# Performance work log

Measured on AMD Instinct MI355X. Metric: run time of the kernel, lower is better.

The kernel has to match this reference:

```python
import jax, jax.numpy as jnp
import numpy as np

T, B, I, H = 512, 128, 512, 1024


def setup_inputs() -> dict:
    key = jax.random.key(0)
    ks = jax.random.split(key, 9)
    stdv = 1.0 / np.sqrt(H).astype(np.float32)
    u = lambda k, shape: jax.random.uniform(k, shape, jnp.float32, -stdv, stdv)
    return {
        "x": jax.random.normal(ks[0], (T, B, I), jnp.float32),
        "Wf": u(ks[1], (H, H + I)), "bf": u(ks[2], (H,)),
        "Wi": u(ks[3], (H, H + I)), "bi": u(ks[4], (H,)),
        "Wc": u(ks[5], (H, H + I)), "bc": u(ks[6], (H,)),
        "Wo": u(ks[7], (H, H + I)), "bo": u(ks[8], (H,)),
    }


def reference(x, Wf, bf, Wi, bi, Wc, bc, Wo, bo):
    # Single-layer unidirectional LSTM (colah equations), scan over time.
    hidden = Wf.shape[0]
    batch = x.shape[1]

    def step(carry, xt):
        h, c = carry
        z = jnp.concatenate([h, xt], axis=-1)          # (B, H+I)
        f = jax.nn.sigmoid(z @ Wf.T + bf)              # forget gate
        i = jax.nn.sigmoid(z @ Wi.T + bi)              # input gate
        c_tilde = jnp.tanh(z @ Wc.T + bc)              # candidate cell
        o = jax.nn.sigmoid(z @ Wo.T + bo)              # output gate
        c_new = f * c + i * c_tilde
        h_new = o * jnp.tanh(c_new)
        return (h_new, c_new), h_new

    h0 = jnp.zeros((batch, hidden), x.dtype)
    c0 = jnp.zeros((batch, hidden), x.dtype)
    (_, _), hs = jax.lax.scan(step, (h0, c0), x)       # hs: (T, B, H)
    return hs
```

## Files before the change

### kernel.cpp

```cpp
#include <hip/hip_runtime.h>
#include <hip/hip_fp16.h>

#define TSTEPS 512
#define NB 128
#define NI 512
#define HID 1024
#define NWGS 256

typedef _Float16 __attribute__((ext_vector_type(8))) half8;
typedef float __attribute__((ext_vector_type(16))) floatx16;
typedef float __attribute__((ext_vector_type(4))) float4v;
typedef unsigned __attribute__((ext_vector_type(4))) uint4v;

#define WPACK_OFF 0
#define HB0_OFF   12582912
#define HB1_OFF   12845056
#define BAR_OFF   13107200

#define LDS_PBUF  98304
#define LDS_HSH   135168
#define LDS_TOTAL 137728

__device__ __forceinline__ short f2h(float f) {
  _Float16 h = (_Float16)f;
  return *reinterpret_cast<short*>(&h);
}

__device__ __forceinline__ half8 pack8(float4v a, float4v b) {
  half8 r;
  r[0] = (_Float16)a[0]; r[1] = (_Float16)a[1]; r[2] = (_Float16)a[2]; r[3] = (_Float16)a[3];
  r[4] = (_Float16)b[0]; r[5] = (_Float16)b[1]; r[6] = (_Float16)b[2]; r[7] = (_Float16)b[3];
  return r;
}

__device__ __forceinline__ float sigf(float x) { return 1.f / (1.f + __expf(-x)); }

__device__ __forceinline__ uint4v cp_load4(const unsigned* p) {
  uint4v v;
  asm volatile("global_load_dwordx4 %0, %1, off sc0 sc1" : "=v"(v) : "v"(p) : "memory");
  asm volatile("s_waitcnt vmcnt(0)" ::: "memory");
  return v;
}
__device__ __forceinline__ void cp_store(unsigned* p, unsigned v) {
  asm volatile("global_store_dword %0, %1, off sc0 sc1" :: "v"(p), "v"(v) : "memory");
}
__device__ __forceinline__ unsigned long long sys_load_u64(const unsigned long long* p) {
  return __hip_atomic_load(p, __ATOMIC_RELAXED, __HIP_MEMORY_SCOPE_SYSTEM);
}

__global__ void pack_w(const float* __restrict__ Wf, const float* __restrict__ Wi,
                       const float* __restrict__ Wc, const float* __restrict__ Wo,
                       _Float16* __restrict__ wpack) {
  int idx = blockIdx.x * 256 + threadIdx.x;
  if (idx >= 128 * 96 * 64) return;
  int lane = idx & 63;
  int rest = idx >> 6;
  int kt = rest % 96;
  int hs = rest / 96;
  int n = lane & 31, q = lane >> 5;
  int j = n >> 2, g = n & 3;
  int row = hs * 8 + j;
  int k = kt * 16 + q * 8;
  const float* W = (g == 0) ? Wf : (g == 1) ? Wi : (g == 2) ? Wc : Wo;
  const float* src = W + (size_t)row * 1536 + k;
  _Float16* dst = wpack + (size_t)idx * 8;
  #pragma unroll
  for (int e = 0; e < 8; e++) dst[e] = (_Float16)src[e];
}

__global__ void zero_h(unsigned* __restrict__ hb0, unsigned* __restrict__ bar) {
  int i = blockIdx.x * 256 + threadIdx.x;
  if (i < 65536)
    __hip_atomic_store(&hb0[i], 0u, __ATOMIC_RELAXED, __HIP_MEMORY_SCOPE_SYSTEM);
  if (i < 512)
    __hip_atomic_store(&bar[i], 0u, __ATOMIC_RELAXED, __HIP_MEMORY_SCOPE_SYSTEM);
}

__global__ void __launch_bounds__(256, 1)
lstm_main(const float* __restrict__ x,
          const float* __restrict__ bfv, const float* __restrict__ biv,
          const float* __restrict__ bcv, const float* __restrict__ bov,
          const _Float16* __restrict__ wpack,
          _Float16* __restrict__ hb0, _Float16* __restrict__ hb1,
          unsigned* __restrict__ bar, float* __restrict__ out) {
  extern __shared__ char lds[];
  short* wlds = (short*)lds;
  float* pbuf = (float*)(lds + LDS_PBUF);
  float* hshare = (float*)(lds + LDS_HSH);

  const int tid = threadIdx.x;
  const int lane = tid & 63;
  const int wv = tid >> 6;
  const int hs = blockIdx.x & 127;
  const int mh = blockIdx.x >> 7;

  {
    const uint4* src = (const uint4*)wpack + (size_t)hs * 6144;
    uint4* dst = (uint4*)wlds;
    #pragma unroll
    for (int i = 0; i < 24; i++) dst[i * 256 + tid] = src[i * 256 + tid];
  }

  const int rj = tid & 7;
  const int rm4 = tid >> 3;
  float rbias[4] = {0.f, 0.f, 0.f, 0.f};
  float cstate[4] = {0.f, 0.f, 0.f, 0.f};
  if (tid < 128) {
    int hg = hs * 8 + rj;
    rbias[0] = bfv[hg]; rbias[1] = biv[hg]; rbias[2] = bcv[hg]; rbias[3] = bov[hg];
  }

  const int n32 = lane & 31;
  const int q = lane >> 5;

  __syncthreads();

  for (int t = 0; t < TSTEPS; t++) {
    const _Float16* hrd = (t & 1) ? hb1 : hb0;
    _Float16* hwr = (t & 1) ? hb0 : hb1;

    floatx16 acc0, acc1;
    #pragma unroll
    for (int i = 0; i < 16; i++) { acc0[i] = 0.f; acc1[i] = 0.f; }

    {
      const float* xbase = x + (size_t)t * NB * NI;
      const int r0 = (mh * 2 + 0) * 32 + n32;
      #pragma unroll
      for (int kk = 0; kk < 8; kk++) {
        int xt = wv * 8 + kk;
        half8 bfrag = *(const half8*)(wlds + ((64 + xt) * 64 + lane) * 8);
        const float* xs = xbase + xt * 16 + q * 8;
        float4v xa0 = *(const float4v*)(xs + (size_t)r0 * NI);
        float4v xb0 = *(const float4v*)(xs + (size_t)r0 * NI + 4);
        float4v xa1 = *(const float4v*)(xs + (size_t)(r0 + 32) * NI);
        float4v xb1 = *(const float4v*)(xs + (size_t)(r0 + 32) * NI + 4);
        acc0 = __builtin_amdgcn_mfma_f32_32x32x16_f16(pack8(xa0, xb0), bfrag, acc0, 0, 0, 0);
        acc1 = __builtin_amdgcn_mfma_f32_32x32x16_f16(pack8(xa1, xb1), bfrag, acc1, 0, 0, 0);
      }
    }

    if (t > 0) {
      const unsigned need = (unsigned)t;
      if (tid < 32) {
        const unsigned* p = bar + mh * 128 + tid * 4;
        for (;;) {
          uint4v v = cp_load4(p);
          int ok = (v[0] >= need) & (v[1] >= need) & (v[2] >= need) & (v[3] >= need);
          unsigned long long b = __ballot(ok);
          if ((unsigned)b == 0xFFFFFFFFu) break;
          __builtin_amdgcn_s_sleep(2);
        }
      }
      __syncthreads();
    }

    {
      const char* hp = (const char*)hrd + ((size_t)mh << 17);
      #pragma unroll
      for (int ph = 0; ph < 2; ph++) {
        unsigned long long w[8][4];
        #pragma unroll
        for (int kk = 0; kk < 8; kk++) {
          int ht = wv * 16 + ph * 8 + kk;
          const unsigned long long* hq =
              (const unsigned long long*)(hp + (((ht * 2 + q) << 10) | (n32 << 4)));
          w[kk][0] = sys_load_u64(hq + 0);
          w[kk][1] = sys_load_u64(hq + 1);
          w[kk][2] = sys_load_u64(hq + 64);
          w[kk][3] = sys_load_u64(hq + 65);
        }
        #pragma unroll
        for (int kk = 0; kk < 8; kk++) {
          int ht = wv * 16 + ph * 8 + kk;
          half8 bfrag = *(const half8*)(wlds + (ht * 64 + lane) * 8);
          union { unsigned long long u[2]; half8 h; } ua, ub;
          ua.u[0] = w[kk][0]; ua.u[1] = w[kk][1];
          ub.u[0] = w[kk][2]; ub.u[1] = w[kk][3];
          acc0 = __builtin_amdgcn_mfma_f32_32x32x16_f16(ua.h, bfrag, acc0, 0, 0, 0);
          acc1 = __builtin_amdgcn_mfma_f32_32x32x16_f16(ub.h, bfrag, acc1, 0, 0, 0);
        }
      }
    }

    {
      float* b0 = pbuf + ((wv * 2 + 0) * 32 + n32) * 36 + q * 4;
      float* b1 = pbuf + ((wv * 2 + 1) * 32 + n32) * 36 + q * 4;
      #pragma unroll
      for (int rg = 0; rg < 4; rg++) {
        float4v v0 = {acc0[rg * 4 + 0], acc0[rg * 4 + 1], acc0[rg * 4 + 2], acc0[rg * 4 + 3]};
        float4v v1 = {acc1[rg * 4 + 0], acc1[rg * 4 + 1], acc1[rg * 4 + 2], acc1[rg * 4 + 3]};
        *(float4v*)(b0 + rg * 8) = v0;
        *(float4v*)(b1 + rg * 8) = v1;
      }
    }
    __syncthreads();

    if (tid < 128) {
      const int mt = rm4 >> 3;
      const int mb = (rm4 & 7) * 4;
      float4v s[4];
      #pragma unroll
      for (int g = 0; g < 4; g++) {
        const float* p = pbuf + (mt * 32 + rj * 4 + g) * 36 + mb;
        float4v a = *(const float4v*)(p);
        a += *(const float4v*)(p + 1 * 2 * 32 * 36);
        a += *(const float4v*)(p + 2 * 2 * 32 * 36);
        a += *(const float4v*)(p + 3 * 2 * 32 * 36);
        s[g] = a;
      }
      #pragma unroll
      for (int r = 0; r < 4; r++) {
        float fg = sigf(s[0][r] + rbias[0]);
        float ig = sigf(s[1][r] + rbias[1]);
        float cg = tanhf(s[2][r] + rbias[2]);
        float og = sigf(s[3][r] + rbias[3]);
        float cn = fg * cstate[r] + ig * cg;
        cstate[r] = cn;
        hshare[(rm4 * 4 + r) * 10 + rj] = og * tanhf(cn);
      }
    }
    __syncthreads();

    {
      const int ml = tid >> 2;
      const int j0 = (tid & 3) * 2;
      float h0 = hshare[ml * 10 + j0];
      float h1 = hshare[ml * 10 + j0 + 1];

      unsigned u = ((unsigned)(unsigned short)f2h(h1) << 16) | (unsigned)(unsigned short)f2h(h0);
      unsigned* dst = (unsigned*)((char*)hwr + (((mh * 128 + hs) << 10))) + tid;
      cp_store(dst, u);

      const int mg = mh * 64 + ml;
      const int hg = hs * 8 + j0;
      *(float2*)(out + ((size_t)t * NB + mg) * HID + hg) = make_float2(h0, h1);
    }

    if (t < TSTEPS - 1) {
      __syncthreads();
      if (tid == 0) {
        asm volatile("s_waitcnt vmcnt(0)" ::: "memory");
        cp_store(&bar[blockIdx.x], (unsigned)(t + 1));
      }
    }
  }
}

extern "C" void kernel_launch(void* const* d_in, const int* in_sizes, int n_in,
                              void* d_out, int out_size, void* d_ws, size_t ws_size,
                              hipStream_t stream) {
  const float* x   = (const float*)d_in[0];
  const float* Wf  = (const float*)d_in[1];
  const float* bf_ = (const float*)d_in[2];
  const float* Wi  = (const float*)d_in[3];
  const float* bi_ = (const float*)d_in[4];
  const float* Wc  = (const float*)d_in[5];
  const float* bc_ = (const float*)d_in[6];
  const float* Wo  = (const float*)d_in[7];
  const float* bo_ = (const float*)d_in[8];
  float* out = (float*)d_out;

  char* ws = (char*)d_ws;
  _Float16* wpack = (_Float16*)(ws + WPACK_OFF);
  _Float16* hb0   = (_Float16*)(ws + HB0_OFF);
  _Float16* hb1   = (_Float16*)(ws + HB1_OFF);
  unsigned* bar   = (unsigned*)(ws + BAR_OFF);

  pack_w<<<3072, 256, 0, stream>>>(Wf, Wi, Wc, Wo, wpack);
  zero_h<<<257, 256, 0, stream>>>((unsigned*)hb0, bar);

  hipFuncSetAttribute(reinterpret_cast<const void*>(lstm_main),
                      hipFuncAttributeMaxDynamicSharedMemorySize, LDS_TOTAL);

  void* args[] = {(void*)&x, (void*)&bf_, (void*)&bi_, (void*)&bc_, (void*)&bo_,
                  (void*)&wpack, (void*)&hb0, (void*)&hb1, (void*)&bar, (void*)&out};
  hipLaunchCooperativeKernel(reinterpret_cast<void*>(lstm_main),
                             dim3(NWGS), dim3(256), args, LDS_TOTAL, stream);
}
```

Baseline: 4.732 ms.

## Distribute barrier polling across waves, prefetch next x, spread gate math over all threads

Each wave now polls its own 32 barrier slots directly with single-dword loads, replacing one wave polling four slots per lane followed by a __syncthreads. The next timestep's x rows are touched after the wait to warm the cache before the next step. The gate and cell update now runs on all 256 threads with two rows each instead of 128 threads with four, cutting the serial transcendental work per thread. The trade-offs are more polling traffic and extra loads on the critical path for the prefetch.

```diff
diff --git a/kernel.cpp b/kernel.cpp
--- a/kernel.cpp
+++ b/kernel.cpp
@@ -10,6 +10,7 @@
 typedef _Float16 __attribute__((ext_vector_type(8))) half8;
 typedef float __attribute__((ext_vector_type(16))) floatx16;
 typedef float __attribute__((ext_vector_type(4))) float4v;
+typedef float __attribute__((ext_vector_type(2))) float2v;
 typedef unsigned __attribute__((ext_vector_type(4))) uint4v;
 
 #define WPACK_OFF 0
@@ -35,9 +36,9 @@
 
 __device__ __forceinline__ float sigf(float x) { return 1.f / (1.f + __expf(-x)); }
 
-__device__ __forceinline__ uint4v cp_load4(const unsigned* p) {
-  uint4v v;
-  asm volatile("global_load_dwordx4 %0, %1, off sc0 sc1" : "=v"(v) : "v"(p) : "memory");
+__device__ __forceinline__ unsigned cp_load(const unsigned* p) {
+  unsigned v;
+  asm volatile("global_load_dword %0, %1, off sc0 sc1" : "=v"(v) : "v"(p) : "memory");
   asm volatile("s_waitcnt vmcnt(0)" ::: "memory");
   return v;
 }
@@ -102,16 +103,20 @@
   }
 
   const int rj = tid & 7;
-  const int rm4 = tid >> 3;
-  float rbias[4] = {0.f, 0.f, 0.f, 0.f};
-  float cstate[4] = {0.f, 0.f, 0.f, 0.f};
-  if (tid < 128) {
+  const int rm8 = tid >> 3;
+  const int rmt = rm8 >> 4;
+  const int rmb = (rm8 & 15) * 2;
+  float rbias[4];
+  float cstate[2] = {0.f, 0.f};
+  {
     int hg = hs * 8 + rj;
     rbias[0] = bfv[hg]; rbias[1] = biv[hg]; rbias[2] = bcv[hg]; rbias[3] = bov[hg];
   }
 
   const int n32 = lane & 31;
   const int q = lane >> 5;
+
+  const unsigned* myslot = bar + mh * 128 + wv * 32 + (lane & 31);
 
   __syncthreads();
 
@@ -142,17 +147,20 @@
 
     if (t > 0) {
       const unsigned need = (unsigned)t;
-      if (tid < 32) {
-        const unsigned* p = bar + mh * 128 + tid * 4;
-        for (;;) {
-          uint4v v = cp_load4(p);
-          int ok = (v[0] >= need) & (v[1] >= need) & (v[2] >= need) & (v[3] >= need);
-          unsigned long long b = __ballot(ok);
-          if ((unsigned)b == 0xFFFFFFFFu) break;
-          __builtin_amdgcn_s_sleep(2);
-        }
-      }
-      __syncthreads();
+      for (;;) {
+        unsigned v = cp_load(myslot);
+        if (__all((int)(v >= need))) break;
+        __builtin_amdgcn_s_sleep(1);
+      }
+    }
+
+    if (t + 1 < TSTEPS) {
+      const float* xn = x + (size_t)(t + 1) * NB * NI + (size_t)mh * 64 * NI;
+      #pragma unroll
+      for (int k = 0; k < 4; k++) {
+        float d = xn[(size_t)(k * 256 + tid) * 32];
+        asm volatile("" :: "v"(d));
+      }
     }
 
     {
@@ -196,28 +204,26 @@
     }
     __syncthreads();
 
-    if (tid < 128) {
-      const int mt = rm4 >> 3;
-      const int mb = (rm4 & 7) * 4;
-      float4v s[4];
+    {
+      float2v s[4];
       #pragma unroll
       for (int g = 0; g < 4; g++) {
-        const float* p = pbuf + (mt * 32 + rj * 4 + g) * 36 + mb;
-        float4v a = *(const float4v*)(p);
-        a += *(const float4v*)(p + 1 * 2 * 32 * 36);
-        a += *(const float4v*)(p + 2 * 2 * 32 * 36);
-        a += *(const float4v*)(p + 3 * 2 * 32 * 36);
+        const float* p = pbuf + (rmt * 32 + rj * 4 + g) * 36 + rmb;
+        float2v a = *(const float2v*)(p);
+        a += *(const float2v*)(p + 1 * 2 * 32 * 36);
+        a += *(const float2v*)(p + 2 * 2 * 32 * 36);
+        a += *(const float2v*)(p + 3 * 2 * 32 * 36);
         s[g] = a;
       }
       #pragma unroll
-      for (int r = 0; r < 4; r++) {
+      for (int r = 0; r < 2; r++) {
         float fg = sigf(s[0][r] + rbias[0]);
         float ig = sigf(s[1][r] + rbias[1]);
         float cg = tanhf(s[2][r] + rbias[2]);
         float og = sigf(s[3][r] + rbias[3]);
         float cn = fg * cstate[r] + ig * cg;
         cstate[r] = cn;
-        hshare[(rm4 * 4 + r) * 10 + rj] = og * tanhf(cn);
+        hshare[(rm8 * 2 + r) * 10 + rj] = og * tanhf(cn);
       }
     }
     __syncthreads();
```

Result: slower. 5.231 ms (+10.5%).
